# Performance work log

Hardware: AMD Instinct MI355X
Metric: run time of the kernel (lower is better)

The kernel has to match this reference:

```python
import jax, jax.numpy as jnp
import numpy as np

TRADE_LAMBDA = 0.25   # trade_lambda
Q = 0.2               # top_bottom_quantile
EPS = 1e-8
LOG_CLAMP = -100.0    # torch BCELoss clamps log terms at -100


def setup_inputs() -> dict:
    key = jax.random.key(0)
    ks = jax.random.split(key, 5)
    B, N = 32, 4096
    scores = jax.random.normal(ks[0], (B, N), jnp.float32)
    # probabilities strictly inside (0,1) for BCE
    p_trade = jax.random.uniform(ks[1], (B, N), jnp.float32, 1e-4, 1.0 - 1e-4)
    y_rank = jax.random.normal(ks[2], (B, N), jnp.float32)
    y_trade = jax.random.uniform(ks[3], (B, N), jnp.float32)
    weights = jax.random.uniform(ks[4], (B, N), jnp.float32, 1e-3, 1.0)
    mask = jnp.ones((B, N), dtype=bool)
    return {"scores": scores, "p_trade": p_trade, "y_rank": y_rank,
            "y_trade": y_trade, "weights": weights, "mask": mask}


def reference(scores, p_trade, y_rank, y_trade, weights, mask):
    B, N = scores.shape
    k = max(1, int(N * Q))  # static per-row top/bottom count (mask is full)

    # ---- L_rank: boolean-weighted pairwise logistic loss ----
    order = jnp.argsort(-y_rank, axis=1)          # descending sort by label, [B, N]
    top = order[:, :k]                            # [B, k] highest-label items
    bot = order[:, -k:]                           # [B, k] lowest-label items
    # meshgrid of (top, bottom) pairs, flattened: [B, k*k]
    idx_i = jnp.broadcast_to(top[:, :, None], (B, k, k)).reshape(B, k * k)
    idx_j = jnp.broadcast_to(bot[:, None, :], (B, k, k)).reshape(B, k * k)

    take = lambda x, idx: jnp.take_along_axis(x, idx, axis=1)
    score_diff = take(scores, idx_i) - take(scores, idx_j)        # [B, k*k]
    w_pair = jnp.sqrt(take(weights, idx_i) * take(weights, idx_j))
    loss_ij = jax.nn.softplus(-score_diff)
    l_rank = (loss_ij * w_pair).sum(axis=1) / (w_pair.sum(axis=1) + EPS)  # [B]

    # ---- L_trade: weighted BCE ----
    log_p = jnp.clip(jnp.log(p_trade), LOG_CLAMP)
    log_1mp = jnp.clip(jnp.log1p(-p_trade), LOG_CLAMP)
    bce = -(y_trade * log_p + (1.0 - y_trade) * log_1mp)          # [B, N]
    wm = weights * mask.astype(weights.dtype)                     # mask as weight (mask is all-true)
    l_trade = (bce * wm).sum(axis=1) / (wm.sum(axis=1) + EPS)     # [B]

    avg_rank = l_rank.mean()
    avg_trade = l_trade.mean()
    total = avg_rank + TRADE_LAMBDA * avg_trade

    maskf = mask.astype(p_trade.dtype)
    mean_p_trade = (p_trade * maskf).sum() / maskf.sum()
    return (total, avg_rank, avg_trade, mean_p_trade)
```

## Files before the change

kernel.cpp:

```cpp
#include <hip/hip_runtime.h>

#define B 32
#define N 4096
#define K 819
#define KP 832
#define SBASE (4*B*KP)
#define JC2 32
#define JL2 26

__device__ __forceinline__ void select_bucket(const int* hist, int R,
                                              int* outBkt, int* outRem) {
  const int lane = threadIdx.x & 63;
  int cnt[32];
  int s = 0;
#pragma unroll
  for (int q = 0; q < 32; q++) { cnt[q] = hist[lane * 32 + q]; s += cnt[q]; }
  int inc = s;
#pragma unroll
  for (int off = 1; off < 64; off <<= 1) {
    int v = __shfl_up(inc, off);
    if (lane >= off) inc += v;
  }
  int exc = inc - s;
  if (R >= exc && R < exc + s) {
    int rem = R - exc, b = 0;
#pragma unroll
    for (int q = 0; q < 32; q++)
      if (b == q && rem >= cnt[q]) { rem -= cnt[q]; b = q + 1; }
    *outBkt = lane * 32 + b;
    *outRem = rem;
  }
}

__device__ __forceinline__ void pick_kth(const float* cand, int c, int rem,
                                         float* out) {
  const int lane = threadIdx.x & 63;
  float v = (lane < c) ? cand[lane] : 3.4e38f;
  int rk = 0;
#pragma unroll 8
  for (int m = 0; m < 64; m++) {
    float u = __shfl(v, m);
    rk += (u < v || (u == v && m < lane)) ? 1 : 0;
  }
  if (lane < c && rk == rem) *out = v;
}

__global__ __launch_bounds__(1024) void wpl_phase1(
    const float* __restrict__ scores, const float* __restrict__ p_trade,
    const float* __restrict__ y_rank, const float* __restrict__ y_trade,
    const float* __restrict__ weights, const unsigned char* __restrict__ mask,
    float* __restrict__ ws) {
  const int r = blockIdx.x;
  const int tid = threadIdx.x;
  __shared__ int hist[2048];
  __shared__ float redMn[16], redMx[16];
  __shared__ float red[16 * 6];
  __shared__ float sMn, sScale, sTlo, sThi;
  __shared__ float candA[64], candB[64];
  __shared__ int cA, cB, cntTop, cntBot;
  __shared__ int bktA, remA, bktB, remB;

  const float4 y4 = ((const float4*)(y_rank  + r * N))[tid];
  const float4 s4 = ((const float4*)(scores  + r * N))[tid];
  const float4 w4 = ((const float4*)(weights + r * N))[tid];
  const float4 p4 = ((const float4*)(p_trade + r * N))[tid];
  const float4 t4 = ((const float4*)(y_trade + r * N))[tid];
  const uchar4 m4 = ((const uchar4*)(mask    + r * N))[tid];
  const float yv[4] = {y4.x, y4.y, y4.z, y4.w};
  const float sv[4] = {s4.x, s4.y, s4.z, s4.w};
  const float wv[4] = {w4.x, w4.y, w4.z, w4.w};
  const float pv[4] = {p4.x, p4.y, p4.z, p4.w};
  const float tv[4] = {t4.x, t4.y, t4.z, t4.w};
  const unsigned char mv[4] = {m4.x, m4.y, m4.z, m4.w};

  hist[tid] = 0; hist[tid + 1024] = 0;
  if (tid == 0) { cA = 0; cB = 0; cntTop = 0; cntBot = 0; }
  float mn = fminf(fminf(yv[0], yv[1]), fminf(yv[2], yv[3]));
  float mx = fmaxf(fmaxf(yv[0], yv[1]), fmaxf(yv[2], yv[3]));
#pragma unroll
  for (int off = 32; off > 0; off >>= 1) {
    mn = fminf(mn, __shfl_down(mn, off));
    mx = fmaxf(mx, __shfl_down(mx, off));
  }
  if ((tid & 63) == 0) { redMn[tid >> 6] = mn; redMx[tid >> 6] = mx; }
  __syncthreads();
  if (tid == 0) {
    float a = redMn[0], b = redMx[0];
    for (int q = 1; q < 16; q++) { a = fminf(a, redMn[q]); b = fmaxf(b, redMx[q]); }
    sMn = a;
    sScale = 2048.0f / (b - a + 1e-20f);
  }
  __syncthreads();

  const float bmn = sMn, bsc = sScale;
#pragma unroll
  for (int q = 0; q < 4; q++) {
    int bkt = (int)((yv[q] - bmn) * bsc);
    bkt = min(2047, max(0, bkt));
    atomicAdd(&hist[bkt], 1);
  }
  __syncthreads();

  if (tid < 64)       select_bucket(hist, K - 1, &bktA, &remA);
  else if (tid < 128) select_bucket(hist, N - K, &bktB, &remB);
  __syncthreads();

  {
    const int bA = bktA, bB = bktB;
#pragma unroll
    for (int q = 0; q < 4; q++) {
      int bkt = (int)((yv[q] - bmn) * bsc);
      bkt = min(2047, max(0, bkt));
      if (bkt == bA) { int p = atomicAdd(&cA, 1); if (p < 64) candA[p] = yv[q]; }
      if (bkt == bB) { int p = atomicAdd(&cB, 1); if (p < 64) candB[p] = yv[q]; }
    }
  }
  __syncthreads();

  if (tid < 64)       pick_kth(candA, cA, remA, &sTlo);
  else if (tid < 128) pick_kth(candB, cB, remB, &sThi);
  __syncthreads();
  const float t_lo = sTlo, t_hi = sThi;

  float2* top = (float2*)ws + (size_t)r * KP;
  float2* bot = (float2*)ws + (size_t)(B + r) * KP;
  if (tid < KP - K) {
    top[K + tid] = make_float2(0.0f, 0.0f);
    bot[K + tid] = make_float2(0.0f, 0.0f);
  }

  float a0 = 0, a1 = 0, a2 = 0, a3 = 0, a4 = 0, a5 = 0;
#pragma unroll
  for (int q = 0; q < 4; q++) {
    float w  = wv[q];
    float sq = sqrtf(w);
    if (yv[q] >= t_hi) {
      int pos = atomicAdd(&cntTop, 1);
      if (pos < K) { top[pos] = make_float2(sv[q], sq); a0 += sq; }
    }
    if (yv[q] <= t_lo) {
      int pos = atomicAdd(&cntBot, 1);
      if (pos < K) { bot[pos] = make_float2(sv[q], sq); a1 += sq; }
    }
    float p  = pv[q];
    float m  = mv[q] ? 1.0f : 0.0f;
    float lp = fmaxf(__logf(p), -100.0f);
    float l1 = fmaxf(log1pf(-p), -100.0f);
    float bce = -(tv[q] * lp + (1.0f - tv[q]) * l1);
    float wm = w * m;
    a2 += bce * wm;
    a3 += wm;
    a4 += p * m;
    a5 += m;
  }

  float vals[6] = {a0, a1, a2, a3, a4, a5};
#pragma unroll
  for (int q = 0; q < 6; q++)
#pragma unroll
    for (int off = 32; off > 0; off >>= 1)
      vals[q] += __shfl_down(vals[q], off);
  const int wave = tid >> 6;
  if ((tid & 63) == 0) {
#pragma unroll
    for (int q = 0; q < 6; q++) red[wave * 6 + q] = vals[q];
  }
  __syncthreads();
  if (tid < 6) {
    float t = 0;
    for (int w2 = 0; w2 < 16; w2++) t += red[w2 * 6 + tid];
    ws[SBASE + tid * B + r] = t;
  }
}

__global__ __launch_bounds__(256) void wpl_phase2(float* __restrict__ ws) {
  const int cj = blockIdx.x;
  const int r  = blockIdx.y;
  const int tid = threadIdx.x;
  __shared__ float2 bsw[JL2];
  __shared__ float red[4];
  const float2* top = (const float2*)ws + (size_t)r * KP;
  const float2* bot = (const float2*)ws + (size_t)(B + r) * KP;
  if (tid < JL2) bsw[tid] = bot[cj * JL2 + tid];
  __syncthreads();

  float acc = 0.0f;
#pragma unroll
  for (int q = 0; q < 4; q++) {
    const int i = q * 256 + tid;
    float2 sw = (i < KP) ? top[i] : make_float2(0.0f, 0.0f);
    float a = 0.0f;
#pragma unroll
    for (int j = 0; j < JL2; j++) {
      float z  = bsw[j].x - sw.x;
      float sp = fmaxf(z, 0.0f) + __logf(1.0f + __expf(-fabsf(z)));
      a += sp * bsw[j].y;
    }
    acc += a * sw.y;
  }
#pragma unroll
  for (int off = 32; off > 0; off >>= 1) acc += __shfl_down(acc, off);
  if ((tid & 63) == 0) red[tid >> 6] = acc;
  __syncthreads();
  if (tid == 0)
    ws[SBASE + 6 * B + r * JC2 + cj] = red[0] + red[1] + red[2] + red[3];
}

__global__ __launch_bounds__(64) void wpl_phase3(const float* __restrict__ ws,
                                                 float* __restrict__ out) {
  const int tid = threadIdx.x;
  float lr = 0, lt = 0, ps = 0, ms = 0;
  if (tid < B) {
    const float* pp = ws + SBASE + 6 * B + tid * JC2;
    float num = 0;
#pragma unroll
    for (int q = 0; q < JC2; q++) num += pp[q];
    float den = ws[SBASE + 0 * B + tid] * ws[SBASE + 1 * B + tid] + 1e-8f;
    lr = num / den;
    lt = ws[SBASE + 2 * B + tid] / (ws[SBASE + 3 * B + tid] + 1e-8f);
    ps = ws[SBASE + 4 * B + tid];
    ms = ws[SBASE + 5 * B + tid];
  }
#pragma unroll
  for (int off = 32; off > 0; off >>= 1) {
    lr += __shfl_down(lr, off);
    lt += __shfl_down(lt, off);
    ps += __shfl_down(ps, off);
    ms += __shfl_down(ms, off);
  }
  if (tid == 0) {
    float avg_rank  = lr * (1.0f / B);
    float avg_trade = lt * (1.0f / B);
    out[0] = avg_rank + 0.25f * avg_trade;
    out[1] = avg_rank;
    out[2] = avg_trade;
    out[3] = ps / ms;
  }
}

extern "C" void kernel_launch(void* const* d_in, const int* in_sizes, int n_in,
                              void* d_out, int out_size, void* d_ws, size_t ws_size,
                              hipStream_t stream) {
  const float* scores  = (const float*)d_in[0];
  const float* p_trade = (const float*)d_in[1];
  const float* y_rank  = (const float*)d_in[2];
  const float* y_trade = (const float*)d_in[3];
  const float* weights = (const float*)d_in[4];
  const unsigned char* mask = (const unsigned char*)d_in[5];
  float* out = (float*)d_out;
  float* ws  = (float*)d_ws;

  wpl_phase1<<<B, 1024, 0, stream>>>(scores, p_trade, y_rank, y_trade, weights, mask, ws);
  wpl_phase2<<<dim3(JC2, B), 256, 0, stream>>>(ws);
  wpl_phase3<<<1, 64, 0, stream>>>(ws, out);
}
```

Baseline: 92.78 us.

## Split threshold selection from row reduction and fold final reduce into pair kernel

Phase 1 is split in two. A threshold kernel reads only y_rank, selects the per-row cut values, and zeroes the accumulators. A reduce kernel then spreads the per-row compaction and BCE sums over 8 chunks per row, using global atomics for counters and sums. The final scalar reduction moves into the pair kernel through a last-block ticket, which removes the third launch. Exchanged for this: y_rank is read twice, global atomic traffic increases, and float-atomic ordering makes the sums nondeterministic.

```diff
diff --git a/kernel.cpp b/kernel.cpp
--- a/kernel.cpp
+++ b/kernel.cpp
@@ -7,6 +7,7 @@
 #define SBASE (4*B*KP)
 #define JC2 32
 #define JL2 26
+#define S_SLOT(s, r) (SBASE + (s)*B + (r))
 
 __device__ __forceinline__ void select_bucket(const int* hist, int R,
                                               int* outBkt, int* outRem) {
@@ -45,27 +46,98 @@
   if (lane < c && rk == rem) *out = v;
 }
 
-__global__ __launch_bounds__(1024) void wpl_phase1(
+__global__ __launch_bounds__(1024) void wpl_thresh(
+    const float* __restrict__ y_rank, float* __restrict__ ws) {
+  const int r = blockIdx.x;
+  const int tid = threadIdx.x;
+  __shared__ int hist[2048];
+  __shared__ float redMn[16], redMx[16];
+  __shared__ float sMn, sScale, sTlo, sThi;
+  __shared__ float candA[64], candB[64];
+  __shared__ int cA, cB, bktA, remA, bktB, remB;
+
+  const float4 y4 = ((const float4*)(y_rank + r * N))[tid];
+  const float yv[4] = {y4.x, y4.y, y4.z, y4.w};
+
+  if (tid < 7) ws[S_SLOT(tid, r)] = 0.0f;
+  else if (tid < 9) ws[S_SLOT(tid + 2, r)] = 0.0f;
+  else if (r == 0 && tid == 9) ((int*)ws)[SBASE + 11 * B] = 0;
+  {
+    float2* top = (float2*)ws + (size_t)r * KP;
+    float2* bot = (float2*)ws + (size_t)(B + r) * KP;
+    if (tid < KP - K) {
+      top[K + tid] = make_float2(0.0f, 0.0f);
+      bot[K + tid] = make_float2(0.0f, 0.0f);
+    }
+  }
+
+  hist[tid] = 0; hist[tid + 1024] = 0;
+  if (tid == 0) { cA = 0; cB = 0; }
+  float mn = fminf(fminf(yv[0], yv[1]), fminf(yv[2], yv[3]));
+  float mx = fmaxf(fmaxf(yv[0], yv[1]), fmaxf(yv[2], yv[3]));
+#pragma unroll
+  for (int off = 32; off > 0; off >>= 1) {
+    mn = fminf(mn, __shfl_down(mn, off));
+    mx = fmaxf(mx, __shfl_down(mx, off));
+  }
+  if ((tid & 63) == 0) { redMn[tid >> 6] = mn; redMx[tid >> 6] = mx; }
+  __syncthreads();
+  if (tid == 0) {
+    float a = redMn[0], b = redMx[0];
+    for (int q = 1; q < 16; q++) { a = fminf(a, redMn[q]); b = fmaxf(b, redMx[q]); }
+    sMn = a;
+    sScale = 2048.0f / (b - a + 1e-20f);
+  }
+  __syncthreads();
+
+  const float bmn = sMn, bsc = sScale;
+#pragma unroll
+  for (int q = 0; q < 4; q++) {
+    int bkt = (int)((yv[q] - bmn) * bsc);
+    atomicAdd(&hist[min(2047, max(0, bkt))], 1);
+  }
+  __syncthreads();
+
+  if (tid < 64)       select_bucket(hist, K - 1, &bktA, &remA);
+  else if (tid < 128) select_bucket(hist, N - K, &bktB, &remB);
+  __syncthreads();
+
+  {
+    const int bA = bktA, bB = bktB;
+#pragma unroll
+    for (int q = 0; q < 4; q++) {
+      int bkt = (int)((yv[q] - bmn) * bsc);
+      bkt = min(2047, max(0, bkt));
+      if (bkt == bA) { int p = atomicAdd(&cA, 1); if (p < 64) candA[p] = yv[q]; }
+      if (bkt == bB) { int p = atomicAdd(&cB, 1); if (p < 64) candB[p] = yv[q]; }
+    }
+  }
+  __syncthreads();
+
+  if (tid < 64)       pick_kth(candA, cA, remA, &sTlo);
+  else if (tid < 128) pick_kth(candB, cB, remB, &sThi);
+  __syncthreads();
+  if (tid == 0) { ws[S_SLOT(7, r)] = sTlo; ws[S_SLOT(8, r)] = sThi; }
+}
+
+__global__ __launch_bounds__(128) void wpl_reduce(
     const float* __restrict__ scores, const float* __restrict__ p_trade,
     const float* __restrict__ y_rank, const float* __restrict__ y_trade,
     const float* __restrict__ weights, const unsigned char* __restrict__ mask,
     float* __restrict__ ws) {
-  const int r = blockIdx.x;
+  const int chunk = blockIdx.x;
+  const int r = blockIdx.y;
   const int tid = threadIdx.x;
-  __shared__ int hist[2048];
-  __shared__ float redMn[16], redMx[16];
-  __shared__ float red[16 * 6];
-  __shared__ float sMn, sScale, sTlo, sThi;
-  __shared__ float candA[64], candB[64];
-  __shared__ int cA, cB, cntTop, cntBot;
-  __shared__ int bktA, remA, bktB, remB;
-
-  const float4 y4 = ((const float4*)(y_rank  + r * N))[tid];
-  const float4 s4 = ((const float4*)(scores  + r * N))[tid];
-  const float4 w4 = ((const float4*)(weights + r * N))[tid];
-  const float4 p4 = ((const float4*)(p_trade + r * N))[tid];
-  const float4 t4 = ((const float4*)(y_trade + r * N))[tid];
-  const uchar4 m4 = ((const uchar4*)(mask    + r * N))[tid];
+  const int e0 = chunk * 512 + tid * 4;
+  const size_t base = (size_t)r * N + e0;
+  __shared__ float red[2 * 6];
+
+  const float4 y4 = *(const float4*)(y_rank  + base);
+  const float4 s4 = *(const float4*)(scores  + base);
+  const float4 w4 = *(const float4*)(weights + base);
+  const float4 p4 = *(const float4*)(p_trade + base);
+  const float4 t4 = *(const float4*)(y_trade + base);
+  const uchar4 m4 = *(const uchar4*)(mask + base);
   const float yv[4] = {y4.x, y4.y, y4.z, y4.w};
   const float sv[4] = {s4.x, s4.y, s4.z, s4.w};
   const float wv[4] = {w4.x, w4.y, w4.z, w4.w};
@@ -73,61 +145,12 @@
   const float tv[4] = {t4.x, t4.y, t4.z, t4.w};
   const unsigned char mv[4] = {m4.x, m4.y, m4.z, m4.w};
 
-  hist[tid] = 0; hist[tid + 1024] = 0;
-  if (tid == 0) { cA = 0; cB = 0; cntTop = 0; cntBot = 0; }
-  float mn = fminf(fminf(yv[0], yv[1]), fminf(yv[2], yv[3]));
-  float mx = fmaxf(fmaxf(yv[0], yv[1]), fmaxf(yv[2], yv[3]));
-#pragma unroll
-  for (int off = 32; off > 0; off >>= 1) {
-    mn = fminf(mn, __shfl_down(mn, off));
-    mx = fmaxf(mx, __shfl_down(mx, off));
-  }
-  if ((tid & 63) == 0) { redMn[tid >> 6] = mn; redMx[tid >> 6] = mx; }
-  __syncthreads();
-  if (tid == 0) {
-    float a = redMn[0], b = redMx[0];
-    for (int q = 1; q < 16; q++) { a = fminf(a, redMn[q]); b = fmaxf(b, redMx[q]); }
-    sMn = a;
-    sScale = 2048.0f / (b - a + 1e-20f);
-  }
-  __syncthreads();
-
-  const float bmn = sMn, bsc = sScale;
-#pragma unroll
-  for (int q = 0; q < 4; q++) {
-    int bkt = (int)((yv[q] - bmn) * bsc);
-    bkt = min(2047, max(0, bkt));
-    atomicAdd(&hist[bkt], 1);
-  }
-  __syncthreads();
-
-  if (tid < 64)       select_bucket(hist, K - 1, &bktA, &remA);
-  else if (tid < 128) select_bucket(hist, N - K, &bktB, &remB);
-  __syncthreads();
-
-  {
-    const int bA = bktA, bB = bktB;
-#pragma unroll
-    for (int q = 0; q < 4; q++) {
-      int bkt = (int)((yv[q] - bmn) * bsc);
-      bkt = min(2047, max(0, bkt));
-      if (bkt == bA) { int p = atomicAdd(&cA, 1); if (p < 64) candA[p] = yv[q]; }
-      if (bkt == bB) { int p = atomicAdd(&cB, 1); if (p < 64) candB[p] = yv[q]; }
-    }
-  }
-  __syncthreads();
-
-  if (tid < 64)       pick_kth(candA, cA, remA, &sTlo);
-  else if (tid < 128) pick_kth(candB, cB, remB, &sThi);
-  __syncthreads();
-  const float t_lo = sTlo, t_hi = sThi;
-
+  const float t_lo = ws[S_SLOT(7, r)];
+  const float t_hi = ws[S_SLOT(8, r)];
+  int* cntTop = (int*)ws + S_SLOT(9, r);
+  int* cntBot = (int*)ws + S_SLOT(10, r);
   float2* top = (float2*)ws + (size_t)r * KP;
   float2* bot = (float2*)ws + (size_t)(B + r) * KP;
-  if (tid < KP - K) {
-    top[K + tid] = make_float2(0.0f, 0.0f);
-    bot[K + tid] = make_float2(0.0f, 0.0f);
-  }
 
   float a0 = 0, a1 = 0, a2 = 0, a3 = 0, a4 = 0, a5 = 0;
 #pragma unroll
@@ -135,11 +158,11 @@
     float w  = wv[q];
     float sq = sqrtf(w);
     if (yv[q] >= t_hi) {
-      int pos = atomicAdd(&cntTop, 1);
+      int pos = atomicAdd(cntTop, 1);
       if (pos < K) { top[pos] = make_float2(sv[q], sq); a0 += sq; }
     }
     if (yv[q] <= t_lo) {
-      int pos = atomicAdd(&cntBot, 1);
+      int pos = atomicAdd(cntBot, 1);
       if (pos < K) { bot[pos] = make_float2(sv[q], sq); a1 += sq; }
     }
     float p  = pv[q];
@@ -160,25 +183,22 @@
 #pragma unroll
     for (int off = 32; off > 0; off >>= 1)
       vals[q] += __shfl_down(vals[q], off);
-  const int wave = tid >> 6;
   if ((tid & 63) == 0) {
 #pragma unroll
-    for (int q = 0; q < 6; q++) red[wave * 6 + q] = vals[q];
-  }
-  __syncthreads();
-  if (tid < 6) {
-    float t = 0;
-    for (int w2 = 0; w2 < 16; w2++) t += red[w2 * 6 + tid];
-    ws[SBASE + tid * B + r] = t;
-  }
-}
-
-__global__ __launch_bounds__(256) void wpl_phase2(float* __restrict__ ws) {
+    for (int q = 0; q < 6; q++) red[(tid >> 6) * 6 + q] = vals[q];
+  }
+  __syncthreads();
+  if (tid < 6) atomicAdd(&ws[S_SLOT(tid, r)], red[tid] + red[6 + tid]);
+}
+
+__global__ __launch_bounds__(256) void wpl_pair(float* __restrict__ ws,
+                                                float* __restrict__ out) {
   const int cj = blockIdx.x;
   const int r  = blockIdx.y;
   const int tid = threadIdx.x;
   __shared__ float2 bsw[JL2];
   __shared__ float red[4];
+  __shared__ int isLast;
   const float2* top = (const float2*)ws + (size_t)r * KP;
   const float2* bot = (const float2*)ws + (size_t)(B + r) * KP;
   if (tid < JL2) bsw[tid] = bot[cj * JL2 + tid];
@@ -202,39 +222,40 @@
   for (int off = 32; off > 0; off >>= 1) acc += __shfl_down(acc, off);
   if ((tid & 63) == 0) red[tid >> 6] = acc;
   __syncthreads();
-  if (tid == 0)
-    ws[SBASE + 6 * B + r * JC2 + cj] = red[0] + red[1] + red[2] + red[3];
-}
-
-__global__ __launch_bounds__(64) void wpl_phase3(const float* __restrict__ ws,
-                                                 float* __restrict__ out) {
-  const int tid = threadIdx.x;
-  float lr = 0, lt = 0, ps = 0, ms = 0;
-  if (tid < B) {
-    const float* pp = ws + SBASE + 6 * B + tid * JC2;
-    float num = 0;
-#pragma unroll
-    for (int q = 0; q < JC2; q++) num += pp[q];
-    float den = ws[SBASE + 0 * B + tid] * ws[SBASE + 1 * B + tid] + 1e-8f;
-    lr = num / den;
-    lt = ws[SBASE + 2 * B + tid] / (ws[SBASE + 3 * B + tid] + 1e-8f);
-    ps = ws[SBASE + 4 * B + tid];
-    ms = ws[SBASE + 5 * B + tid];
-  }
-#pragma unroll
-  for (int off = 32; off > 0; off >>= 1) {
-    lr += __shfl_down(lr, off);
-    lt += __shfl_down(lt, off);
-    ps += __shfl_down(ps, off);
-    ms += __shfl_down(ms, off);
-  }
   if (tid == 0) {
-    float avg_rank  = lr * (1.0f / B);
-    float avg_trade = lt * (1.0f / B);
-    out[0] = avg_rank + 0.25f * avg_trade;
-    out[1] = avg_rank;
-    out[2] = avg_trade;
-    out[3] = ps / ms;
+    atomicAdd(&ws[S_SLOT(6, r)], red[0] + red[1] + red[2] + red[3]);
+    __threadfence();
+    int ticket = atomicAdd((int*)ws + SBASE + 11 * B, 1);
+    isLast = (ticket == JC2 * B - 1) ? 1 : 0;
+  }
+  __syncthreads();
+
+  if (isLast) {
+    __threadfence();
+    float lr = 0, lt = 0, ps = 0, ms = 0;
+    if (tid < B) {
+      float num = ws[S_SLOT(6, tid)];
+      float den = ws[S_SLOT(0, tid)] * ws[S_SLOT(1, tid)] + 1e-8f;
+      lr = num / den;
+      lt = ws[S_SLOT(2, tid)] / (ws[S_SLOT(3, tid)] + 1e-8f);
+      ps = ws[S_SLOT(4, tid)];
+      ms = ws[S_SLOT(5, tid)];
+    }
+#pragma unroll
+    for (int off = 16; off > 0; off >>= 1) {
+      lr += __shfl_down(lr, off);
+      lt += __shfl_down(lt, off);
+      ps += __shfl_down(ps, off);
+      ms += __shfl_down(ms, off);
+    }
+    if (tid == 0) {
+      float avg_rank  = lr * (1.0f / B);
+      float avg_trade = lt * (1.0f / B);
+      out[0] = avg_rank + 0.25f * avg_trade;
+      out[1] = avg_rank;
+      out[2] = avg_trade;
+      out[3] = ps / ms;
+    }
   }
 }
 
@@ -250,7 +271,8 @@
   float* out = (float*)d_out;
   float* ws  = (float*)d_ws;
 
-  wpl_phase1<<<B, 1024, 0, stream>>>(scores, p_trade, y_rank, y_trade, weights, mask, ws);
-  wpl_phase2<<<dim3(JC2, B), 256, 0, stream>>>(ws);
-  wpl_phase3<<<1, 64, 0, stream>>>(ws, out);
-}
+  wpl_thresh<<<B, 1024, 0, stream>>>(y_rank, ws);
+  wpl_reduce<<<dim3(8, B), 128, 0, stream>>>(scores, p_trade, y_rank, y_trade,
+                                             weights, mask, ws);
+  wpl_pair<<<dim3(JC2, B), 256, 0, stream>>>(ws, out);
+}
```

New measurement: 111.3 us. 20.0% more time.
